# Performance work log

Measured on AMD Instinct MI355X. Metric: run time of the kernel, lower is better.

Reference implementation:

```python
import jax, jax.numpy as jnp
import numpy as np

N = 50000   # nodes
E = 600000  # edges (all relations pooled, tagged by rel id)
D = 128     # in_feats
O = 128     # out_feats
R = 8       # num relations
B = 4       # num bases


def setup_inputs() -> dict:
    key = jax.random.key(0)
    ks = jax.random.split(key, 8)
    x = jax.random.normal(ks[0], (N, D), jnp.float32)
    basis_v = jax.random.normal(ks[1], (B, D, O), jnp.float32) * 0.05  # WeightBasis bases
    coeffs = jax.random.normal(ks[2], (R, B), jnp.float32)            # WeightBasis coefficients
    w_loop = jax.random.normal(ks[3], (D, O), jnp.float32) * 0.05     # self_loop_weight
    bias_p = jnp.zeros((O,), jnp.float32)
    src = jax.random.randint(ks[4], (E,), 0, N, dtype=jnp.int32)
    dst = jax.random.randint(ks[5], (E,), 0, N, dtype=jnp.int32)
    rel = jax.random.randint(ks[6], (E,), 0, R, dtype=jnp.int32)
    return dict(x=x, basis_v=basis_v, coeffs=coeffs, w_loop=w_loop,
                bias_p=bias_p, src=src, dst=dst, rel=rel)


def reference(x, basis_v, coeffs, w_loop, bias_p, src, dst, rel):
    # Basis decomposition: W_r = sum_b coeffs[r,b] * V_b  -> [R, D, O]
    W = jnp.einsum('rb,bdo->rdo', coeffs, basis_v)
    # Pre-transform node features per relation (GraphConv applies weight to src): [R, N, O]
    xt = jnp.einsum('nd,rdo->rno', x, W)
    # norm='right': divide aggregated messages by per-relation in-degree of dst
    seg = rel * N + dst  # combined (relation, dst) segment id
    deg = jax.ops.segment_sum(jnp.ones((E,), x.dtype), seg, num_segments=R * N)
    inv_deg = 1.0 / jnp.maximum(deg, 1.0)
    # Gather transformed src feature per edge, normalize, scatter-add to dst.
    msg = xt[rel, src] * inv_deg[seg][:, None]          # [E, O]
    agg = jax.ops.segment_sum(msg, dst, num_segments=N)  # sum over relations (HeteroGraphConv 'sum')
    # Fused self-loop + bias + activation (_apply)
    out = agg + x @ w_loop + bias_p
    return jax.nn.relu(out)
```

## Files before the change

kernel.cpp:

```cpp
#include <hip/hip_runtime.h>

#define N_NODES 50000
#define E_EDGES 600000
#define D_IN 128
#define O_OUT 128
#define R_REL 8
#define B_BAS 4
#define NB1 98
#define NRT 3125
#define NKC 20
#define BKCAP 8192
#define NRG 1563

#define NB_CONV 6250
#define NB_WT 320

#define CHUNK_A 2048
#define NBA 293

typedef __attribute__((ext_vector_type(8))) short bf16x8;
typedef __attribute__((ext_vector_type(4))) short bf16x4;
typedef __attribute__((ext_vector_type(4))) float f32x4;

static __device__ __forceinline__ unsigned short f2bf(float f) {
    unsigned int u = __float_as_uint(f);
    unsigned int r = (u + 0x7fffu + ((u >> 16) & 1u)) >> 16;
    return (unsigned short)r;
}
static __device__ __forceinline__ float bf2f(unsigned short b) {
    return __uint_as_float(((unsigned int)b) << 16);
}

__global__ __launch_bounds__(256) void prep_kernel(const float* __restrict__ x,
                                                   unsigned short* __restrict__ xb,
                                                   const float* __restrict__ basis_v,
                                                   const float* __restrict__ w_loop,
                                                   unsigned short* __restrict__ Wt2f,
                                                   int* __restrict__ cursor98) {
    int b = blockIdx.x;
    if (b == 0 && threadIdx.x < NB1) cursor98[threadIdx.x] = 0;
    if (b < NB_CONV) {
        int i = (b * 256 + threadIdx.x) * 4;
        float4 v = *(const float4*)&x[i];
        ushort4 o;
        o.x = f2bf(v.x); o.y = f2bf(v.y); o.z = f2bf(v.z); o.w = f2bf(v.w);
        *(ushort4*)&xb[i] = o;
    } else {
        int i = (b - NB_CONV) * 256 + threadIdx.x;
        int j = i & 7, l = (i >> 3) & 63, rest = i >> 9;
        int kc = rest % NKC, ct = rest / NKC;
        int col = ct * 16 + (l & 15);
        int k = kc * 32 + (l >> 4) * 8 + j;
        int r = k >> 7, d = k & 127;
        float v = (r < B_BAS) ? basis_v[((size_t)r * D_IN + d) * O_OUT + col]
                              : w_loop[(size_t)d * O_OUT + col];
        Wt2f[i] = f2bf(v);
    }
}

__global__ __launch_bounds__(256) void binA_kernel(const int* __restrict__ src,
                                                   const int* __restrict__ dst,
                                                   const int* __restrict__ rel,
                                                   int* __restrict__ cursor98,
                                                   unsigned* __restrict__ coarse) {
    __shared__ int hist[NB1];
    __shared__ int base[NB1];
    int t = threadIdx.x;
    if (t < NB1) hist[t] = 0;
    __syncthreads();
    int e0 = blockIdx.x * CHUNK_A;
    for (int i = t; i < CHUNK_A; i += 256) {
        int e = e0 + i;
        if (e < E_EDGES) atomicAdd(&hist[dst[e] >> 9], 1);
    }
    __syncthreads();
    if (t < NB1) {
        int h = hist[t];
        base[t] = h ? atomicAdd(&cursor98[t], h) : 0;
        hist[t] = 0;
    }
    __syncthreads();
    for (int i = t; i < CHUNK_A; i += 256) {
        int e = e0 + i;
        if (e < E_EDGES) {
            int d = dst[e], b = d >> 9;
            int pos = base[b] + atomicAdd(&hist[b], 1);
            coarse[(size_t)b * BKCAP + pos] = (unsigned)src[e] | ((unsigned)rel[e] << 16)
                                            | ((unsigned)(d & 511) << 19);
        }
    }
}

__global__ __launch_bounds__(512) void binB_kernel(const unsigned* __restrict__ coarse,
                                                   const int* __restrict__ cursor98,
                                                   unsigned* __restrict__ epack,
                                                   int* __restrict__ begd,
                                                   int* __restrict__ cntd,
                                                   float* __restrict__ invf) {
    __shared__ int hist[512 * 8];
    __shared__ int s[512];
    __shared__ int lcnt[512];
    int b = blockIdx.x, t = threadIdx.x;
    int d0 = b << 9, d = d0 + t;
    #pragma unroll
    for (int r = 0; r < 8; ++r) hist[t * 8 + r] = 0;
    __syncthreads();
    int cnt = cursor98[b];
    const unsigned* cb = coarse + (size_t)b * BKCAP;
    for (int i = t; i < cnt; i += 512) {
        unsigned p = cb[i];
        atomicAdd(&hist[((p >> 19) & 511) * 8 + ((p >> 16) & 7)], 1);
    }
    __syncthreads();
    int c = 0;
    if (d < N_NODES) {
        #pragma unroll
        for (int r = 0; r < 8; ++r) {
            int h = hist[t * 8 + r];
            c += h;
            invf[d * 8 + r] = 1.0f / (float)max(h, 1);
        }
    }
    s[t] = c;
    __syncthreads();
    #pragma unroll
    for (int off = 1; off < 512; off <<= 1) {
        int add = (t >= off) ? s[t - off] : 0;
        __syncthreads();
        s[t] += add;
        __syncthreads();
    }
    int ex = s[t] - c;
    if (d < N_NODES) {
        begd[d] = b * BKCAP + ex;
        cntd[d] = c;
    }
    lcnt[t] = ex;
    __syncthreads();
    for (int i = t; i < cnt; i += 512) {
        unsigned p = cb[i];
        int dlow = (p >> 19) & 511;
        int pos = atomicAdd(&lcnt[dlow], 1);
        epack[(size_t)b * BKCAP + pos] = p & 0x7ffffu;
    }
}

__global__ __launch_bounds__(256) void segagg_kernel(const unsigned short* __restrict__ xb,
                                                     const int* __restrict__ begd,
                                                     const int* __restrict__ cntd,
                                                     const float* __restrict__ invf,
                                                     const unsigned* __restrict__ epack,
                                                     const float* __restrict__ coeffs,
                                                     unsigned short* __restrict__ yfrag) {
    int d = blockIdx.x * 8 + (threadIdx.x >> 5);
    int l = threadIdx.x & 31;
    int beg = begd[d];
    int n = cntd[d];
    const unsigned* ep = epack + beg;
    float a0[4] = {}, a1[4] = {}, a2[4] = {}, a3[4] = {};
    int k = 0;
    for (; k + 4 <= n; k += 4) {
        unsigned p0 = ep[k], p1 = ep[k + 1], p2 = ep[k + 2], p3 = ep[k + 3];
        int s0 = p0 & 0xffffu, r0 = p0 >> 16;
        int s1 = p1 & 0xffffu, r1 = p1 >> 16;
        int s2 = p2 & 0xffffu, r2 = p2 >> 16;
        int s3 = p3 & 0xffffu, r3 = p3 >> 16;
        bf16x4 v0 = *(const bf16x4*)&xb[(size_t)s0 * D_IN + l * 4];
        bf16x4 v1 = *(const bf16x4*)&xb[(size_t)s1 * D_IN + l * 4];
        bf16x4 v2 = *(const bf16x4*)&xb[(size_t)s2 * D_IN + l * 4];
        bf16x4 v3 = *(const bf16x4*)&xb[(size_t)s3 * D_IN + l * 4];
        float i0 = invf[d * R_REL + r0];
        float i1 = invf[d * R_REL + r1];
        float i2 = invf[d * R_REL + r2];
        float i3 = invf[d * R_REL + r3];
        float4 cA = *(const float4*)&coeffs[r0 * B_BAS];
        float4 cB = *(const float4*)&coeffs[r1 * B_BAS];
        float4 cC = *(const float4*)&coeffs[r2 * B_BAS];
        float4 cD = *(const float4*)&coeffs[r3 * B_BAS];
        cA.x *= i0; cA.y *= i0; cA.z *= i0; cA.w *= i0;
        cB.x *= i1; cB.y *= i1; cB.z *= i1; cB.w *= i1;
        cC.x *= i2; cC.y *= i2; cC.z *= i2; cC.w *= i2;
        cD.x *= i3; cD.y *= i3; cD.z *= i3; cD.w *= i3;
        #pragma unroll
        for (int j = 0; j < 4; ++j) {
            float x0 = bf2f((unsigned short)v0[j]);
            float x1 = bf2f((unsigned short)v1[j]);
            float x2 = bf2f((unsigned short)v2[j]);
            float x3 = bf2f((unsigned short)v3[j]);
            a0[j] += cA.x * x0; a1[j] += cA.y * x0;
            a2[j] += cA.z * x0; a3[j] += cA.w * x0;
            a0[j] += cB.x * x1; a1[j] += cB.y * x1;
            a2[j] += cB.z * x1; a3[j] += cB.w * x1;
            a0[j] += cC.x * x2; a1[j] += cC.y * x2;
            a2[j] += cC.z * x2; a3[j] += cC.w * x2;
            a0[j] += cD.x * x3; a1[j] += cD.y * x3;
            a2[j] += cD.z * x3; a3[j] += cD.w * x3;
        }
    }
    for (; k < n; ++k) {
        unsigned p0 = ep[k];
        int s0 = p0 & 0xffffu, r0 = p0 >> 16;
        bf16x4 v0 = *(const bf16x4*)&xb[(size_t)s0 * D_IN + l * 4];
        float i0 = invf[d * R_REL + r0];
        float4 cA = *(const float4*)&coeffs[r0 * B_BAS];
        cA.x *= i0; cA.y *= i0; cA.z *= i0; cA.w *= i0;
        #pragma unroll
        for (int j = 0; j < 4; ++j) {
            float x0 = bf2f((unsigned short)v0[j]);
            a0[j] += cA.x * x0; a1[j] += cA.y * x0;
            a2[j] += cA.z * x0; a3[j] += cA.w * x0;
        }
    }
    int rt = d >> 4, lrow = d & 15;
    int kc0 = l >> 3, lhi = (l >> 1) & 3, jj = (l & 1) * 4;
    size_t rowbase = (size_t)rt * (NKC * 512);
    #pragma unroll
    for (int b = 0; b < 4; ++b) {
        const float* ab = (b == 0) ? a0 : (b == 1) ? a1 : (b == 2) ? a2 : a3;
        ushort4 o;
        o.x = f2bf(ab[0]); o.y = f2bf(ab[1]); o.z = f2bf(ab[2]); o.w = f2bf(ab[3]);
        size_t addr = rowbase + ((size_t)(b * 4 + kc0) * 64 + lhi * 16 + lrow) * 8 + jj;
        *(ushort4*)&yfrag[addr] = o;
    }
    ushort4 xv = *(const ushort4*)&xb[(size_t)d * D_IN + l * 4];
    size_t addr = rowbase + ((size_t)(16 + kc0) * 64 + lhi * 16 + lrow) * 8 + jj;
    *(ushort4*)&yfrag[addr] = xv;
}

__global__ __launch_bounds__(256) void gemm2_kernel(const unsigned short* __restrict__ yfrag,
                                                    const unsigned short* __restrict__ Wt2f,
                                                    const float* __restrict__ bias,
                                                    float* __restrict__ out) {
    const int w = threadIdx.x >> 6, l = threadIdx.x & 63;
    const int wid = blockIdx.x * 4 + w;
    if (wid >= NRG * 2) return;
    const int g = wid >> 1;
    const int ch = wid & 1;
    const int rt0 = g * 2;
    const int rt1 = (rt0 + 1 < NRT) ? rt0 + 1 : rt0;
    const bool has1 = (rt0 + 1 < NRT);
    const unsigned short* ya0 = yfrag + (size_t)rt0 * (NKC * 512) + l * 8;
    const unsigned short* ya1 = yfrag + (size_t)rt1 * (NKC * 512) + l * 8;
    const unsigned short* wb = Wt2f + (size_t)(ch * 4) * (NKC * 512) + l * 8;
    const int KSTEP = 512;

    f32x4 acc00 = {}, acc01 = {}, acc02 = {}, acc03 = {};
    f32x4 acc10 = {}, acc11 = {}, acc12 = {}, acc13 = {};

#define LA0(kc) (*(const bf16x8*)&ya0[(kc) * KSTEP])
#define LA1(kc) (*(const bf16x8*)&ya1[(kc) * KSTEP])
#define LB(ct, kc) (*(const bf16x8*)&wb[((ct) * NKC + (kc)) * KSTEP])

    bf16x8 aE0 = LA0(0), aE1 = LA1(0);
    bf16x8 bE0 = LB(0, 0), bE1 = LB(1, 0), bE2 = LB(2, 0), bE3 = LB(3, 0);
    bf16x8 aO0 = LA0(1), aO1 = LA1(1);
    bf16x8 bO0 = LB(0, 1), bO1 = LB(1, 1), bO2 = LB(2, 1), bO3 = LB(3, 1);

    #pragma unroll
    for (int kc = 0; kc < NKC; kc += 2) {
        acc00 = __builtin_amdgcn_mfma_f32_16x16x32_bf16(aE0, bE0, acc00, 0, 0, 0);
        acc01 = __builtin_amdgcn_mfma_f32_16x16x32_bf16(aE0, bE1, acc01, 0, 0, 0);
        acc02 = __builtin_amdgcn_mfma_f32_16x16x32_bf16(aE0, bE2, acc02, 0, 0, 0);
        acc03 = __builtin_amdgcn_mfma_f32_16x16x32_bf16(aE0, bE3, acc03, 0, 0, 0);
        acc10 = __builtin_amdgcn_mfma_f32_16x16x32_bf16(aE1, bE0, acc10, 0, 0, 0);
        acc11 = __builtin_amdgcn_mfma_f32_16x16x32_bf16(aE1, bE1, acc11, 0, 0, 0);
        acc12 = __builtin_amdgcn_mfma_f32_16x16x32_bf16(aE1, bE2, acc12, 0, 0, 0);
        acc13 = __builtin_amdgcn_mfma_f32_16x16x32_bf16(aE1, bE3, acc13, 0, 0, 0);
        if (kc + 2 < NKC) {
            aE0 = LA0(kc + 2); aE1 = LA1(kc + 2);
            bE0 = LB(0, kc + 2); bE1 = LB(1, kc + 2);
            bE2 = LB(2, kc + 2); bE3 = LB(3, kc + 2);
        }
        acc00 = __builtin_amdgcn_mfma_f32_16x16x32_bf16(aO0, bO0, acc00, 0, 0, 0);
        acc01 = __builtin_amdgcn_mfma_f32_16x16x32_bf16(aO0, bO1, acc01, 0, 0, 0);
        acc02 = __builtin_amdgcn_mfma_f32_16x16x32_bf16(aO0, bO2, acc02, 0, 0, 0);
        acc03 = __builtin_amdgcn_mfma_f32_16x16x32_bf16(aO0, bO3, acc03, 0, 0, 0);
        acc10 = __builtin_amdgcn_mfma_f32_16x16x32_bf16(aO1, bO0, acc10, 0, 0, 0);
        acc11 = __builtin_amdgcn_mfma_f32_16x16x32_bf16(aO1, bO1, acc11, 0, 0, 0);
        acc12 = __builtin_amdgcn_mfma_f32_16x16x32_bf16(aO1, bO2, acc12, 0, 0, 0);
        acc13 = __builtin_amdgcn_mfma_f32_16x16x32_bf16(aO1, bO3, acc13, 0, 0, 0);
        if (kc + 3 < NKC) {
            aO0 = LA0(kc + 3); aO1 = LA1(kc + 3);
            bO0 = LB(0, kc + 3); bO1 = LB(1, kc + 3);
            bO2 = LB(2, kc + 3); bO3 = LB(3, kc + 3);
        }
    }
#undef LA0
#undef LA1
#undef LB

    const int lr = l & 15, lg = l >> 4;
    #pragma unroll
    for (int ct = 0; ct < 4; ++ct) {
        const f32x4& a0 = (ct == 0) ? acc00 : (ct == 1) ? acc01 : (ct == 2) ? acc02 : acc03;
        const f32x4& a1 = (ct == 0) ? acc10 : (ct == 1) ? acc11 : (ct == 2) ? acc12 : acc13;
        int col = (ch * 4 + ct) * 16 + lr;
        float bv = bias[col];
        #pragma unroll
        for (int i2 = 0; i2 < 4; ++i2) {
            int row0 = rt0 * 16 + lg * 4 + i2;
            out[(size_t)row0 * O_OUT + col] = fmaxf(a0[i2] + bv, 0.f);
        }
        if (has1) {
            #pragma unroll
            for (int i2 = 0; i2 < 4; ++i2) {
                int row1 = rt1 * 16 + lg * 4 + i2;
                out[(size_t)row1 * O_OUT + col] = fmaxf(a1[i2] + bv, 0.f);
            }
        }
    }
}

extern "C" void kernel_launch(void* const* d_in, const int* in_sizes, int n_in,
                              void* d_out, int out_size, void* d_ws, size_t ws_size,
                              hipStream_t stream) {
    (void)in_sizes; (void)n_in; (void)out_size; (void)ws_size;
    const float* x       = (const float*)d_in[0];
    const float* basis_v = (const float*)d_in[1];
    const float* coeffs  = (const float*)d_in[2];
    const float* w_loop  = (const float*)d_in[3];
    const float* bias_p  = (const float*)d_in[4];
    const int*   src     = (const int*)d_in[5];
    const int*   dst     = (const int*)d_in[6];
    const int*   rel     = (const int*)d_in[7];
    float* out = (float*)d_out;

    char* ws = (char*)d_ws;
    unsigned short* Wt2f     = (unsigned short*)(ws);
    unsigned short* xb       = (unsigned short*)(ws + 163840);
    float*          invf     = (float*)(ws + 12963840);
    int*            begd     = (int*)(ws + 14563840);
    int*            cntd     = (int*)(ws + 14763840);
    int*            cursor98 = (int*)(ws + 14963840);
    unsigned*       coarse   = (unsigned*)(ws + 14964864);
    unsigned*       epack    = (unsigned*)(ws + 18176128);
    unsigned short* yfrag    = (unsigned short*)(ws + 21387392);

    prep_kernel<<<NB_CONV + NB_WT, 256, 0, stream>>>(x, xb, basis_v, w_loop, Wt2f, cursor98);
    binA_kernel<<<NBA, 256, 0, stream>>>(src, dst, rel, cursor98, coarse);
    binB_kernel<<<NB1, 512, 0, stream>>>(coarse, cursor98, epack, begd, cntd, invf);
    segagg_kernel<<<N_NODES / 8, 256, 0, stream>>>(xb, begd, cntd, invf, epack, coeffs, yfrag);
    gemm2_kernel<<<(NRG * 2 + 3) / 4, 256, 0, stream>>>(yfrag, Wt2f, bias_p, out);
}
```

Baseline: 101.4 us.

## Merge prep and edge binning into one launch; add nontemporal loads and stores

```diff
diff --git a/kernel.cpp b/kernel.cpp
--- a/kernel.cpp
+++ b/kernel.cpp
@@ -14,13 +14,13 @@
 
 #define NB_CONV 6250
 #define NB_WT 320
-
 #define CHUNK_A 2048
 #define NBA 293
 
 typedef __attribute__((ext_vector_type(8))) short bf16x8;
 typedef __attribute__((ext_vector_type(4))) short bf16x4;
 typedef __attribute__((ext_vector_type(4))) float f32x4;
+typedef __attribute__((ext_vector_type(4))) unsigned short u16x4;
 
 static __device__ __forceinline__ unsigned short f2bf(float f) {
     unsigned int u = __float_as_uint(f);
@@ -31,21 +31,24 @@
     return __uint_as_float(((unsigned int)b) << 16);
 }
 
-__global__ __launch_bounds__(256) void prep_kernel(const float* __restrict__ x,
-                                                   unsigned short* __restrict__ xb,
-                                                   const float* __restrict__ basis_v,
-                                                   const float* __restrict__ w_loop,
-                                                   unsigned short* __restrict__ Wt2f,
-                                                   int* __restrict__ cursor98) {
+__global__ __launch_bounds__(256) void prepbin_kernel(const float* __restrict__ x,
+                                                      unsigned short* __restrict__ xb,
+                                                      const float* __restrict__ basis_v,
+                                                      const float* __restrict__ w_loop,
+                                                      unsigned short* __restrict__ Wt2f,
+                                                      const int* __restrict__ src,
+                                                      const int* __restrict__ dst,
+                                                      const int* __restrict__ rel,
+                                                      int* __restrict__ cursor98,
+                                                      unsigned* __restrict__ coarse) {
     int b = blockIdx.x;
-    if (b == 0 && threadIdx.x < NB1) cursor98[threadIdx.x] = 0;
     if (b < NB_CONV) {
         int i = (b * 256 + threadIdx.x) * 4;
         float4 v = *(const float4*)&x[i];
         ushort4 o;
         o.x = f2bf(v.x); o.y = f2bf(v.y); o.z = f2bf(v.z); o.w = f2bf(v.w);
         *(ushort4*)&xb[i] = o;
-    } else {
+    } else if (b < NB_CONV + NB_WT) {
         int i = (b - NB_CONV) * 256 + threadIdx.x;
         int j = i & 7, l = (i >> 3) & 63, rest = i >> 9;
         int kc = rest % NKC, ct = rest / NKC;
@@ -55,38 +58,32 @@
         float v = (r < B_BAS) ? basis_v[((size_t)r * D_IN + d) * O_OUT + col]
                               : w_loop[(size_t)d * O_OUT + col];
         Wt2f[i] = f2bf(v);
-    }
-}
-
-__global__ __launch_bounds__(256) void binA_kernel(const int* __restrict__ src,
-                                                   const int* __restrict__ dst,
-                                                   const int* __restrict__ rel,
-                                                   int* __restrict__ cursor98,
-                                                   unsigned* __restrict__ coarse) {
-    __shared__ int hist[NB1];
-    __shared__ int base[NB1];
-    int t = threadIdx.x;
-    if (t < NB1) hist[t] = 0;
-    __syncthreads();
-    int e0 = blockIdx.x * CHUNK_A;
-    for (int i = t; i < CHUNK_A; i += 256) {
-        int e = e0 + i;
-        if (e < E_EDGES) atomicAdd(&hist[dst[e] >> 9], 1);
-    }
-    __syncthreads();
-    if (t < NB1) {
-        int h = hist[t];
-        base[t] = h ? atomicAdd(&cursor98[t], h) : 0;
-        hist[t] = 0;
-    }
-    __syncthreads();
-    for (int i = t; i < CHUNK_A; i += 256) {
-        int e = e0 + i;
-        if (e < E_EDGES) {
-            int d = dst[e], b = d >> 9;
-            int pos = base[b] + atomicAdd(&hist[b], 1);
-            coarse[(size_t)b * BKCAP + pos] = (unsigned)src[e] | ((unsigned)rel[e] << 16)
-                                            | ((unsigned)(d & 511) << 19);
+    } else {
+        __shared__ int hist[NB1];
+        __shared__ int base[NB1];
+        int t = threadIdx.x;
+        if (t < NB1) hist[t] = 0;
+        __syncthreads();
+        int e0 = (b - NB_CONV - NB_WT) * CHUNK_A;
+        for (int i = t; i < CHUNK_A; i += 256) {
+            int e = e0 + i;
+            if (e < E_EDGES) atomicAdd(&hist[dst[e] >> 9], 1);
+        }
+        __syncthreads();
+        if (t < NB1) {
+            int h = hist[t];
+            base[t] = h ? atomicAdd(&cursor98[t], h) : 0;
+            hist[t] = 0;
+        }
+        __syncthreads();
+        for (int i = t; i < CHUNK_A; i += 256) {
+            int e = e0 + i;
+            if (e < E_EDGES) {
+                int d = dst[e], bb = d >> 9;
+                int pos = base[bb] + atomicAdd(&hist[bb], 1);
+                coarse[(size_t)bb * BKCAP + pos] = (unsigned)src[e] | ((unsigned)rel[e] << 16)
+                                                 | ((unsigned)(d & 511) << 19);
+            }
         }
     }
 }
@@ -217,14 +214,14 @@
     #pragma unroll
     for (int b = 0; b < 4; ++b) {
         const float* ab = (b == 0) ? a0 : (b == 1) ? a1 : (b == 2) ? a2 : a3;
-        ushort4 o;
+        u16x4 o;
         o.x = f2bf(ab[0]); o.y = f2bf(ab[1]); o.z = f2bf(ab[2]); o.w = f2bf(ab[3]);
         size_t addr = rowbase + ((size_t)(b * 4 + kc0) * 64 + lhi * 16 + lrow) * 8 + jj;
-        *(ushort4*)&yfrag[addr] = o;
-    }
-    ushort4 xv = *(const ushort4*)&xb[(size_t)d * D_IN + l * 4];
+        __builtin_nontemporal_store(o, (u16x4*)&yfrag[addr]);
+    }
+    u16x4 xv = *(const u16x4*)&xb[(size_t)d * D_IN + l * 4];
     size_t addr = rowbase + ((size_t)(16 + kc0) * 64 + lhi * 16 + lrow) * 8 + jj;
-    *(ushort4*)&yfrag[addr] = xv;
+    __builtin_nontemporal_store(xv, (u16x4*)&yfrag[addr]);
 }
 
 __global__ __launch_bounds__(256) void gemm2_kernel(const unsigned short* __restrict__ yfrag,
@@ -247,8 +244,8 @@
     f32x4 acc00 = {}, acc01 = {}, acc02 = {}, acc03 = {};
     f32x4 acc10 = {}, acc11 = {}, acc12 = {}, acc13 = {};
 
-#define LA0(kc) (*(const bf16x8*)&ya0[(kc) * KSTEP])
-#define LA1(kc) (*(const bf16x8*)&ya1[(kc) * KSTEP])
+#define LA0(kc) __builtin_nontemporal_load((const bf16x8*)&ya0[(kc) * KSTEP])
+#define LA1(kc) __builtin_nontemporal_load((const bf16x8*)&ya1[(kc) * KSTEP])
 #define LB(ct, kc) (*(const bf16x8*)&wb[((ct) * NKC + (kc)) * KSTEP])
 
     bf16x8 aE0 = LA0(0), aE1 = LA1(0);
@@ -299,13 +296,15 @@
         #pragma unroll
         for (int i2 = 0; i2 < 4; ++i2) {
             int row0 = rt0 * 16 + lg * 4 + i2;
-            out[(size_t)row0 * O_OUT + col] = fmaxf(a0[i2] + bv, 0.f);
+            __builtin_nontemporal_store(fmaxf(a0[i2] + bv, 0.f),
+                                        &out[(size_t)row0 * O_OUT + col]);
         }
         if (has1) {
             #pragma unroll
             for (int i2 = 0; i2 < 4; ++i2) {
                 int row1 = rt1 * 16 + lg * 4 + i2;
-                out[(size_t)row1 * O_OUT + col] = fmaxf(a1[i2] + bv, 0.f);
+                __builtin_nontemporal_store(fmaxf(a1[i2] + bv, 0.f),
+                                            &out[(size_t)row1 * O_OUT + col]);
             }
         }
     }
@@ -336,8 +335,9 @@
     unsigned*       epack    = (unsigned*)(ws + 18176128);
     unsigned short* yfrag    = (unsigned short*)(ws + 21387392);
 
-    prep_kernel<<<NB_CONV + NB_WT, 256, 0, stream>>>(x, xb, basis_v, w_loop, Wt2f, cursor98);
-    binA_kernel<<<NBA, 256, 0, stream>>>(src, dst, rel, cursor98, coarse);
+    hipMemsetAsync(cursor98, 0, NB1 * sizeof(int), stream);
+    prepbin_kernel<<<NB_CONV + NB_WT + NBA, 256, 0, stream>>>(x, xb, basis_v, w_loop, Wt2f,
+                                                              src, dst, rel, cursor98, coarse);
     binB_kernel<<<NB1, 512, 0, stream>>>(coarse, cursor98, epack, begd, cntd, invf);
     segagg_kernel<<<N_NODES / 8, 256, 0, stream>>>(xb, begd, cntd, invf, epack, coeffs, yfrag);
     gemm2_kernel<<<(NRG * 2 + 3) / 4, 256, 0, stream>>>(yfrag, Wt2f, bias_p, out);
```

Measured after the change: 156.5 us. +54.3%, slower.
